# Kernel tuning notes

Measured on AMD Instinct MI355X. Metric: run time of the kernel, lower is better.

The kernel has to match this reference:

```python
import jax, jax.numpy as jnp
import numpy as np

B, C1, C2, D, NH, H, W = 2, 64, 256, 256, 8, 64, 64
HD = D // NH
EPS = 1e-5


def setup_inputs() -> dict:
    key = jax.random.key(0)
    ks = jax.random.split(key, 12)
    s = lambda fan_in: 1.0 / np.sqrt(fan_in)
    return {
        "F_lidar": jax.random.normal(ks[0], (B, C1, H, W), jnp.float32),
        "F_cam": jax.random.normal(ks[1], (B, C2, H, W), jnp.float32),
        "Wq": jax.random.normal(ks[2], (D, C1), jnp.float32) * s(C1),
        "Wk": jax.random.normal(ks[3], (D, C2), jnp.float32) * s(C2),
        "Wv": jax.random.normal(ks[4], (D, C2), jnp.float32) * s(C2),
        "Wo": jax.random.normal(ks[5], (D, D), jnp.float32) * s(D),
        "Wres": jax.random.normal(ks[6], (D, C1), jnp.float32) * s(C1),
        "g1": jnp.ones((D,), jnp.float32),
        "b1": jnp.zeros((D,), jnp.float32),
        "g2": jnp.ones((D,), jnp.float32),
        "b2": jnp.zeros((D,), jnp.float32),
        "W1": jax.random.normal(ks[7], (4 * D, D), jnp.float32) * s(D),
        "bf1": jnp.zeros((4 * D,), jnp.float32),
        "W2": jax.random.normal(ks[8], (D, 4 * D), jnp.float32) * s(4 * D),
        "bf2": jnp.zeros((D,), jnp.float32),
    }


def _layernorm(x, g, b):
    mu = jnp.mean(x, axis=-1, keepdims=True)
    var = jnp.mean(jnp.square(x - mu), axis=-1, keepdims=True)
    return (x - mu) * jax.lax.rsqrt(var + EPS) * g + b


def reference(F_lidar, F_cam, Wq, Wk, Wv, Wo, Wres, g1, b1, g2, b2, W1, bf1, W2, bf2):
    b, _, h, w = F_lidar.shape
    n = h * w
    # channels-last token views: (B, HW, C)
    xl = F_lidar.reshape(b, C1, n).transpose(0, 2, 1)
    xc = F_cam.reshape(b, C2, n).transpose(0, 2, 1)
    # 1x1 conv projections == per-token matmuls
    Q = jnp.einsum('bnc,dc->bnd', xl, Wq).reshape(b, n, NH, HD).transpose(0, 2, 1, 3)
    K = jnp.einsum('bnc,dc->bnd', xc, Wk).reshape(b, n, NH, HD).transpose(0, 2, 1, 3)
    V = jnp.einsum('bnc,dc->bnd', xc, Wv).reshape(b, n, NH, HD).transpose(0, 2, 1, 3)
    scale = HD ** -0.5
    scores = jnp.einsum('bhqd,bhkd->bhqk', Q, K) * scale  # (B,NH,HW,HW)
    attn = jax.nn.softmax(scores, axis=-1)
    out = jnp.einsum('bhqk,bhkd->bhqd', attn, V)
    out = out.transpose(0, 2, 1, 3).reshape(b, n, D)
    out = jnp.einsum('bnd,ed->bne', out, Wo)
    resid = jnp.einsum('bnc,dc->bnd', xl, Wres)
    x = _layernorm(resid + out, g1, b1)
    # FFN (dropout = identity in eval)
    hdn = jax.nn.relu(jnp.einsum('bnd,fd->bnf', x, W1) + bf1)
    ffn = jnp.einsum('bnf,df->bnd', hdn, W2) + bf2
    x = _layernorm(x + ffn, g2, b2)
    return x.transpose(0, 2, 1).reshape(b, D, h, w)
```

## Files before the change

### kernel.cpp

```cpp
#include <hip/hip_runtime.h>
#include <hip/hip_bf16.h>
#include <math.h>

#define NB 2
#define C1 64
#define C2 256
#define DD 256
#define NHH 8
#define HDD 32
#define NN 4096
#define FF 1024
#define MTOT (NB*NN)
#define KVB 128

typedef unsigned short u16;
typedef __attribute__((ext_vector_type(8))) short bf16x8;
typedef __attribute__((ext_vector_type(4))) float f32x4;
typedef __attribute__((ext_vector_type(4))) unsigned short us4;
typedef __attribute__((ext_vector_type(4))) unsigned int u32x4;

__device__ __forceinline__ u16 f2bf(float f) {
    union { float f; unsigned int i; } u; u.f = f;
    unsigned int r = u.i + 0x7FFFu + ((u.i >> 16) & 1u);
    return (u16)(r >> 16);
}

__device__ __forceinline__ unsigned cvt_pk_bf16(float a, float b) {
    unsigned r; asm("v_cvt_pk_bf16_f32 %0, %1, %2" : "=v"(r) : "v"(a), "v"(b)); return r;
}

__device__ __forceinline__ void glds16(const void* g, void* l) {
    __builtin_amdgcn_global_load_lds(
        (__attribute__((address_space(1))) void*)g,
        (__attribute__((address_space(3))) void*)l, 16, 0, 0);
}

__device__ __forceinline__ void tconv_body(const float* __restrict__ src,
    u16* __restrict__ dst, int C, int n0, int c0, int b, int t,
    float (*tile)[65])
{
#pragma unroll
    for (int i = 0; i < 4; ++i) {
        int cc = t + i * 256;
        int c = cc >> 4, off = (cc & 15) * 4;
        const float4 v = *(const float4*)&src[((size_t)b*C + c0 + c)*NN + n0 + off];
        tile[c][off+0] = v.x; tile[c][off+1] = v.y;
        tile[c][off+2] = v.z; tile[c][off+3] = v.w;
    }
    __syncthreads();
    const int n = t >> 2, cch = (t & 3) * 16;
    bf16x8 t0, t1;
#pragma unroll
    for (int i = 0; i < 8; ++i) ((u16*)&t0)[i] = f2bf(tile[cch + i][n]);
#pragma unroll
    for (int i = 0; i < 8; ++i) ((u16*)&t1)[i] = f2bf(tile[cch + 8 + i][n]);
    u16* dp = &dst[((size_t)b*NN + n0 + n)*C + c0 + cch];
    *(bf16x8*)&dp[0] = t0;
    *(bf16x8*)&dp[8] = t1;
}

__global__ __launch_bounds__(256) void prep(
    const float* __restrict__ Wq, const float* __restrict__ Wres,
    const float* __restrict__ Wk, const float* __restrict__ Wv,
    const float* __restrict__ Wo, const float* __restrict__ W1,
    const float* __restrict__ W2, u16* __restrict__ d,
    const float* __restrict__ F_lidar, const float* __restrict__ F_cam,
    u16* __restrict__ xl, u16* __restrict__ xc)
{
    __shared__ float tile[64][65];
    const int id = blockIdx.x, t = threadIdx.x;
    if (id < 736) {
        int i4 = (id * 256 + t) * 4;
        const float* s; int off;
        if      (i4 <  16384) { s = Wq;   off = i4; }
        else if (i4 <  32768) { s = Wres; off = i4 -  16384; }
        else if (i4 <  98304) { s = Wk;   off = i4 -  32768; }
        else if (i4 < 163840) { s = Wv;   off = i4 -  98304; }
        else if (i4 < 229376) { s = Wo;   off = i4 - 163840; }
        else if (i4 < 491520) { s = W1;   off = i4 - 229376; }
        else                  { s = W2;   off = i4 - 491520; }
        const float4 v = *(const float4*)&s[off];
        us4 o; o[0] = f2bf(v.x); o[1] = f2bf(v.y); o[2] = f2bf(v.z); o[3] = f2bf(v.w);
        *(us4*)&d[i4] = o;
    } else if (id < 864) {
        int l = id - 736;
        tconv_body(F_lidar, xl, C1, (l & 63)*64, 0, l >> 6, t, tile);
    } else {
        int l = id - 864;
        tconv_body(F_cam, xc, C2, (l & 63)*64, ((l >> 6) & 3)*64, l >> 8, t, tile);
    }
}

template<int MODE, int BM>
__device__ __forceinline__ void gemm_body(
    const u16* __restrict__ A, const u16* __restrict__ Bw,
    int N, int K,
    const float* __restrict__ bias, const float* __restrict__ add,
    float* __restrict__ outf, u16* __restrict__ outb, float scale,
    int bm, int bn, u16* lA, u16* lB)
{
    constexpr int MFR = BM / 32;
    constexpr int ASZ = BM * 32;
    const int t = threadIdx.x, lane = t & 63, wid = t >> 6;
    const int wr = (wid >> 1) * (BM/2), wc = (wid & 1) * 64;
    const int lrow = lane & 15, lk = (lane >> 4) * 8;
    const int arow = wid*(BM/4) + (lane >> 2);
    const int brow = wid*32 + (lane >> 2);
    const int soff = (lane & 3) * 8;
    const u16* aS = &A[(size_t)(bm + arow)*K + soff];
    const u16* bS = &Bw[(size_t)(bn + brow)*K + soff];
    const int lwA = wid*(BM/4)*32;
    const int lwB = wid*1024;
    f32x4 acc[MFR][4] = {};

    glds16(aS, &lA[lwA]);
    if (BM == 128) glds16(aS + (size_t)16*K, &lA[lwA + 512]);
    glds16(bS, &lB[lwB]);
    glds16(bS + (size_t)16*K, &lB[lwB + 512]);
    __syncthreads();

    const int nst = K >> 5;
    for (int st = 0; st < nst; ++st) {
        const int cur = st & 1;
        if (st < nst - 1) {
            const int k0 = (st + 1) * 32;
            const int nb = (cur ^ 1);
            glds16(aS + k0, &lA[nb*ASZ + lwA]);
            if (BM == 128) glds16(aS + (size_t)16*K + k0, &lA[nb*ASZ + lwA + 512]);
            glds16(bS + k0, &lB[nb*4096 + lwB]);
            glds16(bS + (size_t)16*K + k0, &lB[nb*4096 + lwB + 512]);
        }
        bf16x8 af[MFR], bfr[4];
#pragma unroll
        for (int mf = 0; mf < MFR; ++mf)
            af[mf] = *(const bf16x8*)&lA[cur*ASZ + (wr + mf*16 + lrow)*32 + lk];
#pragma unroll
        for (int nf = 0; nf < 4; ++nf)
            bfr[nf] = *(const bf16x8*)&lB[cur*4096 + (wc + nf*16 + lrow)*32 + lk];
#pragma unroll
        for (int mf = 0; mf < MFR; ++mf)
#pragma unroll
            for (int nf = 0; nf < 4; ++nf)
                acc[mf][nf] = __builtin_amdgcn_mfma_f32_16x16x32_bf16(af[mf], bfr[nf], acc[mf][nf], 0, 0, 0);
        __syncthreads();
    }
#pragma unroll
    for (int mf = 0; mf < MFR; ++mf) {
#pragma unroll
        for (int nf = 0; nf < 4; ++nf) {
#pragma unroll
            for (int j = 0; j < 4; ++j) {
                int row = bm + wr + mf*16 + (lane >> 4)*4 + j;
                int col = bn + wc + nf*16 + lrow;
                float v = acc[mf][nf][j];
                if (MODE == 0) {
                    size_t idx = (size_t)row*N + col;
                    outf[idx] = v + add[idx];
                } else if (MODE == 1) {
                    float r = v + bias[col];
                    outb[(size_t)row*N + col] = f2bf(r > 0.f ? r : 0.f);
                } else if (MODE == 2) {
                    size_t idx = (size_t)row*N + col;
                    outf[idx] = v + bias[col] + add[idx];
                } else if (MODE == 3) {
                    int b = row >> 12, n = row & 4095;
                    if (col < 256) {
                        int h = col >> 5, hd = col & 31;
                        int bh = b*NHH + h;
                        size_t idx = (((size_t)bh*256 + (n >> 4))*64
                                      + (hd >> 3)*16 + (n & 15))*8 + (hd & 7);
                        outb[idx] = f2bf(v);
                    } else {
                        int c = col - 256;
                        int h = c >> 5, hd = c & 31;
                        int hf = hd >> 4, d2 = hd & 15;
                        int bh = b*NHH + h;
                        int kb = n >> 5, kwb = n & 31;
                        int hp = kwb >> 4, gg = (kwb >> 2) & 3, r = kwb & 3;
                        size_t idx = ((((size_t)bh*128 + kb)*2 + hf)*64 + gg*16 + d2)*8
                                   + hp*4 + r;
                        ((u16*)outf)[idx] = f2bf(v);
                    }
                } else {
                    int b = row >> 12, n = row & 4095;
                    if (col < 256) {
                        int h = col >> 5, hd = col & 31;
                        outb[(((size_t)b*NHH + h)*NN + n)*HDD + hd] = f2bf(v * scale);
                    } else {
                        outf[(size_t)row*DD + (col - 256)] = v;
                    }
                }
            }
        }
    }
}

template<int MODE, int BM>
__global__ __launch_bounds__(256) void gemm_bt(
    const u16* __restrict__ A, const u16* __restrict__ Bw,
    int N, int K, const float* __restrict__ bias, const float* __restrict__ add,
    float* __restrict__ outf, u16* __restrict__ outb, float scale)
{
    __shared__ u16 lA[2*BM*32];
    __shared__ u16 lB[2*4096];
    gemm_body<MODE, BM>(A, Bw, N, K, bias, add, outf, outb, scale,
                        blockIdx.x*BM, blockIdx.y*128, lA, lB);
}

__global__ __launch_bounds__(256) void qkv_gemm(
    const u16* __restrict__ xl, const u16* __restrict__ xc,
    const u16* __restrict__ WqRes, const u16* __restrict__ WkWv,
    float* __restrict__ resid, u16* __restrict__ Qb,
    u16* __restrict__ Kperm, u16* __restrict__ Vperm, float qscale)
{
    __shared__ u16 lA[2*128*32];
    __shared__ u16 lB[2*4096];
    int l = blockIdx.x;
    if (l < 256) {
        gemm_body<4, 128>(xl, WqRes, 512, 64, nullptr, nullptr, resid, Qb,
                          qscale, (l & 63)*128, (l >> 6)*128, lA, lB);
    } else {
        l -= 256;
        gemm_body<3, 128>(xc, WkWv, 512, 256, nullptr, nullptr,
                          (float*)Vperm, Kperm, 1.f, (l & 63)*128, (l >> 6)*128, lA, lB);
    }
}

__global__ __launch_bounds__(256) void flash_attn(
    const u16* __restrict__ Qp, const u16* __restrict__ Kperm,
    const u16* __restrict__ Vperm, u16* __restrict__ Op)
{
    __shared__ u16 Kl[2][4096];
    __shared__ u16 Vl[2][4096];
    const int id = blockIdx.x;
    const int sw = (id & 7) * 128 + (id >> 3);
    const int qt = sw & 63;
    const int bh = sw >> 6;
    const size_t base = (size_t)bh * NN * HDD;
    const int t = threadIdx.x, lane = t & 63, w = t >> 6;
    const int q0 = qt * 64;
    const int lrow = lane & 15, g = lane >> 4;

    const bf16x8 qf = *(const bf16x8*)&Qp[base + (size_t)(q0 + w*16 + lrow)*HDD + g*8];

    const u16* kgw = &Kperm[(size_t)bh*131072 + w*1024 + lane*8];
    const u16* vgw = &Vperm[(size_t)bh*131072 + w*1024 + lane*8];
    const int lw = w * 1024;

    u32x4 onesw = {0x3F803F80u, 0x3F803F80u, 0x3F803F80u, 0x3F803F80u};
    const bf16x8 ones = *(bf16x8*)&onesw;

    glds16(kgw,       &Kl[0][lw]);
    glds16(kgw + 512, &Kl[0][lw + 512]);
    glds16(vgw,       &Vl[0][lw]);
    glds16(vgw + 512, &Vl[0][lw + 512]);

    f32x4 o[2] = {};
    f32x4 osum = {};
    __syncthreads();

#define FLASH_STEP(CUR, TT)                                                    \
    {                                                                          \
        if ((TT) < 31) {                                                       \
            const u16* kg = kgw + (size_t)((TT)+1)*4096;                       \
            const u16* vg = vgw + (size_t)((TT)+1)*4096;                       \
            glds16(kg,       &Kl[(CUR)^1][lw]);                                \
            glds16(kg + 512, &Kl[(CUR)^1][lw + 512]);                          \
            glds16(vg,       &Vl[(CUR)^1][lw]);                                \
            glds16(vg + 512, &Vl[(CUR)^1][lw + 512]);                          \
        }                                                                      \
        f32x4 s[8];                                                            \
        __builtin_amdgcn_s_setprio(1);                                         \
        _Pragma("unroll")                                                      \
        for (int nf = 0; nf < 8; ++nf) {                                       \
            bf16x8 kf = *(const bf16x8*)&Kl[(CUR)][nf*512 + lane*8];           \
            f32x4 z = {};                                                      \
            s[nf] = __builtin_amdgcn_mfma_f32_16x16x32_bf16(kf, qf, z, 0, 0, 0); \
        }                                                                      \
        __builtin_amdgcn_s_setprio(0);                                         \
        _Pragma("unroll")                                                      \
        for (int kk = 0; kk < 4; ++kk) {                                       \
            float p0[4], p1[4];                                                \
            _Pragma("unroll")                                                  \
            for (int jj = 0; jj < 4; ++jj) {                                   \
                p0[jj] = __builtin_amdgcn_exp2f(s[2*kk][jj]);                  \
                p1[jj] = __builtin_amdgcn_exp2f(s[2*kk+1][jj]);                 \
            }                                                                  \
            u32x4 paw;                                                         \
            paw[0] = cvt_pk_bf16(p0[0], p0[1]);                                \
            paw[1] = cvt_pk_bf16(p0[2], p0[3]);                                \
            paw[2] = cvt_pk_bf16(p1[0], p1[1]);                                \
            paw[3] = cvt_pk_bf16(p1[2], p1[3]);                                \
            bf16x8 pa = *(bf16x8*)&paw;                                        \
            __builtin_amdgcn_s_setprio(1);                                     \
            _Pragma("unroll")                                                  \
            for (int hf = 0; hf < 2; ++hf) {                                   \
                bf16x8 vf = *(const bf16x8*)&Vl[(CUR)][kk*1024 + hf*512 + lane*8]; \
                o[hf] = __builtin_amdgcn_mfma_f32_16x16x32_bf16(pa, vf, o[hf], 0, 0, 0); \
            }                                                                  \
            osum = __builtin_amdgcn_mfma_f32_16x16x32_bf16(pa, ones, osum, 0, 0, 0); \
            __builtin_amdgcn_s_setprio(0);                                     \
        }                                                                      \
        __syncthreads();                                                       \
    }

    for (int tt = 0; tt < 32; tt += 2) {
        FLASH_STEP(0, tt)
        FLASH_STEP(1, tt + 1)
    }
#undef FLASH_STEP

    const int b = bh >> 3, h = bh & 7;
#pragma unroll
    for (int hf = 0; hf < 2; ++hf)
#pragma unroll
        for (int r = 0; r < 4; ++r) {
            int q = q0 + w*16 + g*4 + r;
            int d = h*HDD + hf*16 + lrow;
            Op[((size_t)b*NN + q)*DD + d] = f2bf(o[hf][r] / osum[r]);
        }
}

__global__ __launch_bounds__(256) void ln_fuse(const float* __restrict__ y,
    const float* __restrict__ g, const float* __restrict__ be,
    float* __restrict__ x, u16* __restrict__ xb)
{
    const int row = blockIdx.x * 4 + (threadIdx.x >> 6);
    const int lane = threadIdx.x & 63;
    const float4 v = *(const float4*)&y[(size_t)row*DD + lane*4];
    float s1 = v.x + v.y + v.z + v.w;
    float s2 = v.x*v.x + v.y*v.y + v.z*v.z + v.w*v.w;
#pragma unroll
    for (int m = 1; m <= 32; m <<= 1) { s1 += __shfl_xor(s1, m); s2 += __shfl_xor(s2, m); }
    float mean = s1 * (1.f/DD);
    float var  = s2 * (1.f/DD) - mean*mean;
    float rstd = rsqrtf(var + 1e-5f);
    const float vv[4] = {v.x, v.y, v.z, v.w};
    float4 xo; us4 xo16;
#pragma unroll
    for (int i = 0; i < 4; ++i) {
        int d = lane*4 + i;
        float r = (vv[i] - mean) * rstd * g[d] + be[d];
        ((float*)&xo)[i] = r;
        xo16[i] = f2bf(r);
    }
    *(float4*)&x[(size_t)row*DD + lane*4] = xo;
    *(us4*)&xb[(size_t)row*DD + lane*4] = xo16;
}

__global__ __launch_bounds__(256) void ln2_transpose(const float* __restrict__ z,
    const float* __restrict__ g, const float* __restrict__ be,
    float* __restrict__ out)
{
    __shared__ float tile[32][257];
    const int n0 = blockIdx.x * 32;
    const int b = blockIdx.y;
    const int t = threadIdx.x, lane = t & 63, w = t >> 6;
    for (int r8 = 0; r8 < 8; ++r8) {
        int r = w*8 + r8;
        const float4 v = *(const float4*)&z[((size_t)b*NN + n0 + r)*DD + lane*4];
        float s1 = v.x + v.y + v.z + v.w;
        float s2 = v.x*v.x + v.y*v.y + v.z*v.z + v.w*v.w;
#pragma unroll
        for (int m = 1; m <= 32; m <<= 1) { s1 += __shfl_xor(s1, m); s2 += __shfl_xor(s2, m); }
        float mean = s1 * (1.f/DD);
        float var  = s2 * (1.f/DD) - mean*mean;
        float rstd = rsqrtf(var + 1e-5f);
        const float vv[4] = {v.x, v.y, v.z, v.w};
#pragma unroll
        for (int i = 0; i < 4; ++i) {
            int d = lane*4 + i;
            tile[r][d] = (vv[i] - mean)*rstd*g[d] + be[d];
        }
    }
    __syncthreads();
    const int n = t & 31, dg = t >> 5;
    for (int dd = 0; dd < 32; ++dd) {
        int d = dd*8 + dg;
        out[((size_t)b*DD + d)*NN + n0 + n] = tile[n][d];
    }
}

extern "C" void kernel_launch(void* const* d_in, const int* in_sizes, int n_in,
                              void* d_out, int out_size, void* d_ws, size_t ws_size,
                              hipStream_t stream)
{
    const float* F_lidar = (const float*)d_in[0];
    const float* F_cam   = (const float*)d_in[1];
    const float* Wq  = (const float*)d_in[2];
    const float* Wk  = (const float*)d_in[3];
    const float* Wv  = (const float*)d_in[4];
    const float* Wo  = (const float*)d_in[5];
    const float* Wrs = (const float*)d_in[6];
    const float* g1  = (const float*)d_in[7];
    const float* b1  = (const float*)d_in[8];
    const float* g2  = (const float*)d_in[9];
    const float* b2  = (const float*)d_in[10];
    const float* W1  = (const float*)d_in[11];
    const float* bf1 = (const float*)d_in[12];
    const float* W2  = (const float*)d_in[13];
    const float* bf2 = (const float*)d_in[14];
    float* out = (float*)d_out;

    char* ws = (char*)d_ws;
    size_t cur = 0;
    auto carve = [&](size_t bytes) {
        size_t o = cur; cur += (bytes + 255) & ~(size_t)255; return (void*)(ws + o);
    };
    u16* wb    = (u16*)carve(753664u * 2);
    u16* xl    = (u16*)carve((size_t)MTOT * C1 * 2);
    u16* xc    = (u16*)carve((size_t)MTOT * C2 * 2);
    u16* Qb    = (u16*)carve((size_t)MTOT * DD * 2);
    u16* Kperm = (u16*)carve((size_t)MTOT * DD * 2);
    u16* Vperm = (u16*)carve((size_t)MTOT * DD * 2);
    float* resid = (float*)carve((size_t)MTOT * DD * 4);
    u16* attn  = (u16*)carve((size_t)MTOT * DD * 2);
    float* y   = (float*)carve((size_t)MTOT * DD * 4);
    float* x   = (float*)carve((size_t)MTOT * DD * 4);
    u16* xb    = (u16*)carve((size_t)MTOT * DD * 2);
    u16* hdn   = (u16*)carve((size_t)MTOT * FF * 2);
    float* zb  = y;

    u16* WqRes = wb;
    u16* WkWv  = wb + 32768;
    u16* Wob   = wb + 163840;
    u16* W1b   = wb + 229376;
    u16* W2b   = wb + 491520;

    prep<<<1376, 256, 0, stream>>>(Wq, Wrs, Wk, Wv, Wo, W1, W2, wb,
                                   F_lidar, F_cam, xl, xc);

    const float qscale = 1.4426950408889634f / sqrtf((float)HDD);
    qkv_gemm<<<512, 256, 0, stream>>>(xl, xc, WqRes, WkWv,
                                      resid, Qb, Kperm, Vperm, qscale);

    flash_attn<<<1024, 256, 0, stream>>>(Qb, Kperm, Vperm, attn);

    gemm_bt<0, 64><<<dim3(128, 2), 256, 0, stream>>>(attn, Wob, DD, DD,
        nullptr, resid, y, nullptr, 1.f);
    ln_fuse<<<2048, 256, 0, stream>>>(y, g1, b1, x, xb);
    gemm_bt<1, 128><<<dim3(64, 8), 256, 0, stream>>>(xb, W1b, FF, DD,
        bf1, nullptr, nullptr, hdn, 1.f);
    gemm_bt<2, 64><<<dim3(128, 2), 256, 0, stream>>>(hdn, W2b, DD, FF,
        bf2, x, zb, nullptr, 1.f);
    ln2_transpose<<<dim3(128, NB), 256, 0, stream>>>(zb, g2, b2, out);
}
```

Baseline: 123.8 us.

## Fuse Wo and W2 GEMMs with LayerNorm epilogues into full-row tile kernels

Adds a gemm_ln kernel that computes a 32-row by full-256-column tile, stages the results in LDS, then applies the residual add, bias, and LayerNorm in the epilogue. The second variant also performs the channel-first transpose store. This removes the fp32 intermediate y/z round trips and two extra launches (ln_fuse, ln2_transpose). In exchange, the two GEMMs now launch only 256 blocks with small 32-row tiles, which may lower MFMA efficiency. The W2 GEMM now carries a K=1024 loop per block.

```diff
diff --git a/kernel.cpp b/kernel.cpp
--- a/kernel.cpp
+++ b/kernel.cpp
@@ -153,15 +153,9 @@
                 int row = bm + wr + mf*16 + (lane >> 4)*4 + j;
                 int col = bn + wc + nf*16 + lrow;
                 float v = acc[mf][nf][j];
-                if (MODE == 0) {
-                    size_t idx = (size_t)row*N + col;
-                    outf[idx] = v + add[idx];
-                } else if (MODE == 1) {
+                if (MODE == 1) {
                     float r = v + bias[col];
                     outb[(size_t)row*N + col] = f2bf(r > 0.f ? r : 0.f);
-                } else if (MODE == 2) {
-                    size_t idx = (size_t)row*N + col;
-                    outf[idx] = v + bias[col] + add[idx];
                 } else if (MODE == 3) {
                     int b = row >> 12, n = row & 4095;
                     if (col < 256) {
@@ -181,7 +175,7 @@
                                    + hp*4 + r;
                         ((u16*)outf)[idx] = f2bf(v);
                     }
-                } else {
+                } else if (MODE == 4) {
                     int b = row >> 12, n = row & 4095;
                     if (col < 256) {
                         int h = col >> 5, hd = col & 31;
@@ -223,6 +217,119 @@
         l -= 256;
         gemm_body<3, 128>(xc, WkWv, 512, 256, nullptr, nullptr,
                           (float*)Vperm, Kperm, 1.f, (l & 63)*128, (l >> 6)*128, lA, lB);
+    }
+}
+
+template<int MODE>
+__global__ __launch_bounds__(256) void gemm_ln(
+    const u16* __restrict__ A, const u16* __restrict__ Bw, int K,
+    const float* __restrict__ bias, const float* __restrict__ add,
+    const float* __restrict__ g, const float* __restrict__ be,
+    float* __restrict__ xf, u16* __restrict__ xb, float* __restrict__ out)
+{
+    __shared__ char smem[37888];
+    u16* lA = (u16*)smem;
+    u16* lB = (u16*)(smem + 4096);
+    float (*epi)[257] = (float(*)[257])smem;
+
+    const int bm = blockIdx.x * 32;
+    const int t = threadIdx.x, lane = t & 63, wid = t >> 6;
+    const int wc = wid * 64;
+    const int lrow = lane & 15, g4 = lane >> 4, lk = g4 * 8;
+    const int sr = lane >> 2, sc = (lane & 3) * 8;
+    const u16* aS = &A[(size_t)(bm + wid*16 + sr)*K + sc];
+    const u16* bS = &Bw[(size_t)(wid*64 + sr)*K + sc];
+    f32x4 acc[2][4] = {};
+
+    if (wid < 2) glds16(aS, &lA[wid*512]);
+#pragma unroll
+    for (int c = 0; c < 4; ++c)
+        glds16(bS + (size_t)c*16*K, &lB[wid*2048 + c*512]);
+    __syncthreads();
+
+    const int nst = K >> 5;
+    for (int st = 0; st < nst; ++st) {
+        const int cur = st & 1;
+        if (st < nst - 1) {
+            const int k0 = (st + 1) * 32;
+            const int nb = cur ^ 1;
+            if (wid < 2) glds16(aS + k0, &lA[nb*1024 + wid*512]);
+#pragma unroll
+            for (int c = 0; c < 4; ++c)
+                glds16(bS + (size_t)c*16*K + k0, &lB[nb*8192 + wid*2048 + c*512]);
+        }
+        bf16x8 af[2], bfr[4];
+#pragma unroll
+        for (int mf = 0; mf < 2; ++mf)
+            af[mf] = *(const bf16x8*)&lA[cur*1024 + (mf*16 + lrow)*32 + lk];
+#pragma unroll
+        for (int nf = 0; nf < 4; ++nf)
+            bfr[nf] = *(const bf16x8*)&lB[cur*8192 + (wc + nf*16 + lrow)*32 + lk];
+#pragma unroll
+        for (int mf = 0; mf < 2; ++mf)
+#pragma unroll
+            for (int nf = 0; nf < 4; ++nf)
+                acc[mf][nf] = __builtin_amdgcn_mfma_f32_16x16x32_bf16(af[mf], bfr[nf], acc[mf][nf], 0, 0, 0);
+        __syncthreads();
+    }
+
+#pragma unroll
+    for (int mf = 0; mf < 2; ++mf)
+#pragma unroll
+        for (int nf = 0; nf < 4; ++nf)
+#pragma unroll
+            for (int j = 0; j < 4; ++j) {
+                int rl = mf*16 + g4*4 + j;
+                int col = wc + nf*16 + lrow;
+                float v = acc[mf][nf][j];
+                if (MODE == 0) v += add[(size_t)(bm + rl)*DD + col];
+                else           v += bias[col] + add[(size_t)(bm + rl)*DD + col];
+                epi[rl][col] = v;
+            }
+    __syncthreads();
+
+#pragma unroll
+    for (int r8 = 0; r8 < 8; ++r8) {
+        int r = wid*8 + r8;
+        const float4 v = *(const float4*)&epi[r][lane*4];
+        float s1 = v.x + v.y + v.z + v.w;
+        float s2 = v.x*v.x + v.y*v.y + v.z*v.z + v.w*v.w;
+#pragma unroll
+        for (int m = 1; m <= 32; m <<= 1) { s1 += __shfl_xor(s1, m); s2 += __shfl_xor(s2, m); }
+        float mean = s1 * (1.f/DD);
+        float var  = s2 * (1.f/DD) - mean*mean;
+        float rstd = rsqrtf(var + 1e-5f);
+        const float vv[4] = {v.x, v.y, v.z, v.w};
+        if (MODE == 0) {
+            float4 xo; us4 xo16;
+#pragma unroll
+            for (int i = 0; i < 4; ++i) {
+                int d = lane*4 + i;
+                float rr = (vv[i] - mean) * rstd * g[d] + be[d];
+                ((float*)&xo)[i] = rr;
+                xo16[i] = f2bf(rr);
+            }
+            *(float4*)&xf[(size_t)(bm + r)*DD + lane*4] = xo;
+            *(us4*)&xb[(size_t)(bm + r)*DD + lane*4] = xo16;
+        } else {
+            float4 xo;
+#pragma unroll
+            for (int i = 0; i < 4; ++i) {
+                int d = lane*4 + i;
+                ((float*)&xo)[i] = (vv[i] - mean) * rstd * g[d] + be[d];
+            }
+            *(float4*)&epi[r][lane*4] = xo;
+        }
+    }
+    if (MODE == 1) {
+        __syncthreads();
+        const int n = t & 31, dg = t >> 5;
+        const int b = bm >> 12, n0 = bm & 4095;
+#pragma unroll
+        for (int dd = 0; dd < 32; ++dd) {
+            int d = dd*8 + dg;
+            out[((size_t)b*DD + d)*NN + n0 + n] = epi[n][d];
+        }
     }
 }
 
@@ -321,66 +428,6 @@
         }
 }
 
-__global__ __launch_bounds__(256) void ln_fuse(const float* __restrict__ y,
-    const float* __restrict__ g, const float* __restrict__ be,
-    float* __restrict__ x, u16* __restrict__ xb)
-{
-    const int row = blockIdx.x * 4 + (threadIdx.x >> 6);
-    const int lane = threadIdx.x & 63;
-    const float4 v = *(const float4*)&y[(size_t)row*DD + lane*4];
-    float s1 = v.x + v.y + v.z + v.w;
-    float s2 = v.x*v.x + v.y*v.y + v.z*v.z + v.w*v.w;
-#pragma unroll
-    for (int m = 1; m <= 32; m <<= 1) { s1 += __shfl_xor(s1, m); s2 += __shfl_xor(s2, m); }
-    float mean = s1 * (1.f/DD);
-    float var  = s2 * (1.f/DD) - mean*mean;
-    float rstd = rsqrtf(var + 1e-5f);
-    const float vv[4] = {v.x, v.y, v.z, v.w};
-    float4 xo; us4 xo16;
-#pragma unroll
-    for (int i = 0; i < 4; ++i) {
-        int d = lane*4 + i;
-        float r = (vv[i] - mean) * rstd * g[d] + be[d];
-        ((float*)&xo)[i] = r;
-        xo16[i] = f2bf(r);
-    }
-    *(float4*)&x[(size_t)row*DD + lane*4] = xo;
-    *(us4*)&xb[(size_t)row*DD + lane*4] = xo16;
-}
-
-__global__ __launch_bounds__(256) void ln2_transpose(const float* __restrict__ z,
-    const float* __restrict__ g, const float* __restrict__ be,
-    float* __restrict__ out)
-{
-    __shared__ float tile[32][257];
-    const int n0 = blockIdx.x * 32;
-    const int b = blockIdx.y;
-    const int t = threadIdx.x, lane = t & 63, w = t >> 6;
-    for (int r8 = 0; r8 < 8; ++r8) {
-        int r = w*8 + r8;
-        const float4 v = *(const float4*)&z[((size_t)b*NN + n0 + r)*DD + lane*4];
-        float s1 = v.x + v.y + v.z + v.w;
-        float s2 = v.x*v.x + v.y*v.y + v.z*v.z + v.w*v.w;
-#pragma unroll
-        for (int m = 1; m <= 32; m <<= 1) { s1 += __shfl_xor(s1, m); s2 += __shfl_xor(s2, m); }
-        float mean = s1 * (1.f/DD);
-        float var  = s2 * (1.f/DD) - mean*mean;
-        float rstd = rsqrtf(var + 1e-5f);
-        const float vv[4] = {v.x, v.y, v.z, v.w};
-#pragma unroll
-        for (int i = 0; i < 4; ++i) {
-            int d = lane*4 + i;
-            tile[r][d] = (vv[i] - mean)*rstd*g[d] + be[d];
-        }
-    }
-    __syncthreads();
-    const int n = t & 31, dg = t >> 5;
-    for (int dd = 0; dd < 32; ++dd) {
-        int d = dd*8 + dg;
-        out[((size_t)b*DD + d)*NN + n0 + n] = tile[n][d];
-    }
-}
-
 extern "C" void kernel_launch(void* const* d_in, const int* in_sizes, int n_in,
                               void* d_out, int out_size, void* d_ws, size_t ws_size,
                               hipStream_t stream)
@@ -415,11 +462,9 @@
     u16* Vperm = (u16*)carve((size_t)MTOT * DD * 2);
     float* resid = (float*)carve((size_t)MTOT * DD * 4);
     u16* attn  = (u16*)carve((size_t)MTOT * DD * 2);
-    float* y   = (float*)carve((size_t)MTOT * DD * 4);
     float* x   = (float*)carve((size_t)MTOT * DD * 4);
     u16* xb    = (u16*)carve((size_t)MTOT * DD * 2);
     u16* hdn   = (u16*)carve((size_t)MTOT * FF * 2);
-    float* zb  = y;
 
     u16* WqRes = wb;
     u16* WkWv  = wb + 32768;
@@ -436,12 +481,10 @@
 
     flash_attn<<<1024, 256, 0, stream>>>(Qb, Kperm, Vperm, attn);
 
-    gemm_bt<0, 64><<<dim3(128, 2), 256, 0, stream>>>(attn, Wob, DD, DD,
-        nullptr, resid, y, nullptr, 1.f);
-    ln_fuse<<<2048, 256, 0, stream>>>(y, g1, b1, x, xb);
+    gemm_ln<0><<<256, 256, 0, stream>>>(attn, Wob, DD,
+        nullptr, resid, g1, b1, x, xb, nullptr);
     gemm_bt<1, 128><<<dim3(64, 8), 256, 0, stream>>>(xb, W1b, FF, DD,
         bf1, nullptr, nullptr, hdn, 1.f);
-    gemm_bt<2, 64><<<dim3(128, 2), 256, 0, stream>>>(hdn, W2b, DD, FF,
-        bf2, x, zb, nullptr, 1.f);
-    ln2_transpose<<<dim3(128, NB), 256, 0, stream>>>(zb, g2, b2, out);
-}
+    gemm_ln<1><<<256, 256, 0, stream>>>(hdn, W2b, FF,
+        bf2, x, g2, b2, nullptr, nullptr, out);
+}
```

Result: no change. 122.2 us (-1.3%).
